# Kernel tuning notes

Measured on AMD Instinct MI355X. Metric: run time of the kernel, lower is better.

The kernel has to match this reference:

```python
import jax, jax.numpy as jnp
import numpy as np

N_NODES = 100000
N_EDGES = 1600000
D_IN, D_HID, D_LAT = 128, 128, 64


def setup_inputs() -> dict:
    key = jax.random.key(0)
    ks = jax.random.split(key, 8)
    x = jax.random.normal(ks[0], (N_NODES, D_IN), dtype=jnp.float32)
    edge_index = jax.random.randint(ks[1], (2, N_EDGES), 0, N_NODES, dtype=jnp.int64)
    s1 = 1.0 / np.sqrt(D_IN)
    s2 = 1.0 / np.sqrt(D_HID)
    return {
        "x": x,
        "edge_index": edge_index,
        "W1_l": jax.random.normal(ks[2], (D_IN, D_HID), dtype=jnp.float32) * s1,
        "W1_r": jax.random.normal(ks[3], (D_IN, D_HID), dtype=jnp.float32) * s1,
        "b1": jnp.zeros((D_HID,), dtype=jnp.float32),
        "W2_l": jax.random.normal(ks[4], (D_HID, D_LAT), dtype=jnp.float32) * s2,
        "W2_r": jax.random.normal(ks[5], (D_HID, D_LAT), dtype=jnp.float32) * s2,
        "b2": jnp.zeros((D_LAT,), dtype=jnp.float32),
    }


def _sage_conv_mean(x, src, dst, W_l, W_r, b):
    """PyG SAGEConv with mean aggregation: lin_l(mean_j x_j) + lin_r(x_i)."""
    n = x.shape[0]
    # scatter-mean of source features into destination nodes
    agg = jax.ops.segment_sum(x[src], dst, num_segments=n)           # [N, d]
    deg = jax.ops.segment_sum(jnp.ones_like(dst, dtype=x.dtype), dst, num_segments=n)
    mean = agg / jnp.maximum(deg, 1.0)[:, None]
    return mean @ W_l + b + x @ W_r


def reference(x, edge_index, W1_l, W1_r, b1, W2_l, W2_r, b2):
    src, dst = edge_index[0], edge_index[1]
    h = jax.nn.relu(_sage_conv_mean(x, src, dst, W1_l, W1_r, b1))
    # Dropout(p=0.2) is identity in eval mode
    z = jax.nn.relu(_sage_conv_mean(h, src, dst, W2_l, W2_r, b2))
    return z
```

## Files before the change

kernel.cpp:

```cpp
#include <hip/hip_runtime.h>

#define N_NODES 100000
#define N_EDGES 1600000
#define D_IN 128
#define D_HID 128
#define D_LAT 64

#define BSHIFT 8
#define NB 392
#define CAP 4608
#define EPB 4096
#define PART_BLOCKS ((N_EDGES + EPB - 1) / EPB)
#define CVT_BLOCKS (((long)N_NODES * 128 / 16 + 255) / 256)

typedef unsigned short ushort_t;
typedef unsigned int uint_t;
typedef unsigned char uchar_t;
using bf16x8 = __attribute__((ext_vector_type(8))) short;
using f32x4  = __attribute__((ext_vector_type(4))) float;
using f32x2  = __attribute__((ext_vector_type(2))) float;

__device__ inline ushort_t f2bf(float f) {
    uint_t u = __float_as_uint(f);
    return (ushort_t)((u + 0x7fffu + ((u >> 16) & 1u)) >> 16);
}
__device__ inline uint_t pack2bf(float a, float b) {
    return (uint_t)f2bf(a) | ((uint_t)f2bf(b) << 16);
}
__device__ inline float bf2f(ushort_t u) {
    return __uint_as_float(((uint_t)u) << 16);
}

#if __has_builtin(__builtin_amdgcn_cvt_pk_f32_fp8) && __has_builtin(__builtin_amdgcn_cvt_pk_fp8_f32)
#define HW_FP8 1
template<bool HI>
__device__ inline f32x2 fp8pk2f(uint_t v) {
    return __builtin_amdgcn_cvt_pk_f32_fp8(v, HI);
}
__device__ inline uint_t f2fp8pk4(float a, float b, float c, float d) {
    uint_t w = __builtin_amdgcn_cvt_pk_fp8_f32(a, b, 0, false);
    w = __builtin_amdgcn_cvt_pk_fp8_f32(c, d, w, true);
    return w;
}
__device__ inline uchar_t f2fp8_byte(float f) {
    return (uchar_t)(__builtin_amdgcn_cvt_pk_fp8_f32(f, f, 0, false) & 0xff);
}
#else
__device__ inline float fp8b2f(uint_t b) {
    uint_t em = b & 0x7f;
    if (em == 0) return 0.f;
    uint_t bits = ((em << 20) + (120u << 23)) | ((b & 0x80u) << 24);
    return __uint_as_float(bits);
}
template<bool HI>
__device__ inline f32x2 fp8pk2f(uint_t v) {
    uint_t w = HI ? (v >> 16) : v;
    f32x2 r; r.x = fp8b2f(w & 0xff); r.y = fp8b2f((w >> 8) & 0xff);
    return r;
}
__device__ inline uint_t f2fp8_1(float f) {
    uint_t u = __float_as_uint(f);
    uint_t s = (u >> 31) << 7;
    uint_t au = u & 0x7fffffff;
    if (au >= 0x43e00000u) return s | 0x7e;
    if (au < 0x3c000000u) return s;
    uint_t r = au + 0x0007ffffu + ((au >> 20) & 1u);
    return s | (((r >> 20) - (120u << 3)) & 0x7f);
}
__device__ inline uint_t f2fp8pk4(float a, float b, float c, float d) {
    return f2fp8_1(a) | (f2fp8_1(b) << 8) | (f2fp8_1(c) << 16) | (f2fp8_1(d) << 24);
}
__device__ inline uchar_t f2fp8_byte(float f) { return (uchar_t)f2fp8_1(f); }
#endif

__device__ inline void accf8x4(float* a, uint_t w, int base) {
    f32x2 p0 = fp8pk2f<false>(w);
    f32x2 p1 = fp8pk2f<true>(w);
    a[base + 0] += p0.x; a[base + 1] += p0.y;
    a[base + 2] += p1.x; a[base + 3] += p1.y;
}
__device__ inline void accf8x16(float* a, uint4 u) {
    accf8x4(a, u.x, 0); accf8x4(a, u.y, 4); accf8x4(a, u.z, 8); accf8x4(a, u.w, 12);
}

template<int RSHIFT>
__device__ inline void gather_acc_fp8(const uchar_t* __restrict__ base,
                                      const int* __restrict__ idxp,
                                      int n, float* acc) {
    int k = 0;
    int idx[8];
    if (n >= 8) {
        #pragma unroll
        for (int j = 0; j < 8; ++j) idx[j] = idxp[j];
    }
    while (k + 8 <= n) {
        uint4 u[8];
        #pragma unroll
        for (int j = 0; j < 8; ++j)
            u[j] = *(const uint4*)(base + ((long)idx[j] << RSHIFT));
        int kn = k + 8;
        if (kn + 8 <= n) {
            #pragma unroll
            for (int j = 0; j < 8; ++j) idx[j] = idxp[kn + j];
        }
        #pragma unroll
        for (int j = 0; j < 8; ++j) accf8x16(acc, u[j]);
        k = kn;
    }
    if (k < n) {
        int m = n - k;
        int idr[8];
        #pragma unroll
        for (int j = 0; j < 8; ++j) {
            int kk = k + j; if (kk > n - 1) kk = n - 1;
            idr[j] = idxp[kk];
        }
        uint4 u[8];
        #pragma unroll
        for (int j = 0; j < 8; ++j)
            u[j] = *(const uint4*)(base + ((long)idr[j] << RSHIFT));
        #pragma unroll
        for (int j = 0; j < 8; ++j) if (j < m) accf8x16(acc, u[j]);
    }
}

__device__ inline void pack_w256(const float* Wl, const float* Wr, ushort_t* pack,
                                 int N, int tid) {
    int lane = tid & 63;
    int t = tid >> 6;
    int kt = t & 7;
    int nt = t >> 3;
    int n = nt * 16 + (lane & 15);
    int kbase = kt * 32 + (lane >> 4) * 8;
    ushort_t v[8];
    #pragma unroll
    for (int j = 0; j < 8; ++j) {
        int k = kbase + j;
        float w = (k < 128) ? Wl[k * N + n] : Wr[(k - 128) * N + n];
        v[j] = f2bf(w);
    }
    *(uint4*)(pack + (long)tid * 8) = *(uint4*)v;
}
__device__ inline void pack_w128(const float* W, ushort_t* pack, int N, int tid) {
    int lane = tid & 63;
    int t = tid >> 6;
    int kt = t & 3;
    int nt = t >> 2;
    int n = nt * 16 + (lane & 15);
    int kbase = kt * 32 + (lane >> 4) * 8;
    ushort_t v[8];
    #pragma unroll
    for (int j = 0; j < 8; ++j) v[j] = f2bf(W[(kbase + j) * N + n]);
    *(uint4*)(pack + (long)tid * 8) = *(uint4*)v;
}

__global__ __launch_bounds__(256) void prep_kernel(
        const float* __restrict__ W1_l, const float* __restrict__ W1_r,
        ushort_t* __restrict__ pack1,
        const float* __restrict__ W2_l, ushort_t* __restrict__ pack2l,
        const float* __restrict__ W2_r, ushort_t* __restrict__ pack2r,
        int* __restrict__ gCur,
        const float* __restrict__ x, ushort_t* __restrict__ xb,
        uchar_t* __restrict__ x8) {
    int b = blockIdx.x;
    if (b < 16) {
        pack_w256(W1_l, W1_r, pack1, 128, b * 256 + threadIdx.x);
    } else if (b < 20) {
        pack_w128(W2_l, pack2l, 64, (b - 16) * 256 + threadIdx.x);
    } else if (b < 24) {
        pack_w128(W2_r, pack2r, 64, (b - 20) * 256 + threadIdx.x);
    } else if (b < 26) {
        int t = (b - 24) * 256 + threadIdx.x;
        if (t < NB) gCur[t] = t * CAP;
    } else {
        long i = ((long)(b - 26) * 256 + threadIdx.x) * 16;
        if (i >= (long)N_NODES * 128) return;
        float4 a = *(const float4*)(x + i);
        float4 bb = *(const float4*)(x + i + 4);
        float4 c = *(const float4*)(x + i + 8);
        float4 d = *(const float4*)(x + i + 12);
        uint4 ob0, ob1;
        ob0.x = pack2bf(a.x, a.y);  ob0.y = pack2bf(a.z, a.w);
        ob0.z = pack2bf(bb.x, bb.y); ob0.w = pack2bf(bb.z, bb.w);
        ob1.x = pack2bf(c.x, c.y);  ob1.y = pack2bf(c.z, c.w);
        ob1.z = pack2bf(d.x, d.y);  ob1.w = pack2bf(d.z, d.w);
        *(uint4*)(xb + i) = ob0;
        *(uint4*)(xb + i + 8) = ob1;
        uint4 o8;
        o8.x = f2fp8pk4(a.x, a.y, a.z, a.w);
        o8.y = f2fp8pk4(bb.x, bb.y, bb.z, bb.w);
        o8.z = f2fp8pk4(c.x, c.y, c.z, c.w);
        o8.w = f2fp8pk4(d.x, d.y, d.z, d.w);
        *(uint4*)(x8 + i) = o8;
    }
}

__global__ __launch_bounds__(256) void bucket_scatter_kernel(const int* __restrict__ src,
                                                             const int* __restrict__ dst,
                                                             int* __restrict__ gCur,
                                                             int* __restrict__ bedges) {
    __shared__ int h[NB];
    __shared__ int start[NB];
    for (int j = threadIdx.x; j < NB; j += 256) h[j] = 0;
    __syncthreads();
    long base = (long)blockIdx.x * EPB + threadIdx.x * 16;
    int dc[16], sc[16];
    int cnt = 0;
    if (base + 16 <= N_EDGES) {
        #pragma unroll
        for (int j = 0; j < 4; ++j) {
            int4 d4 = *(const int4*)(dst + base + j * 4);
            int4 s4 = *(const int4*)(src + base + j * 4);
            dc[j * 4 + 0] = d4.x; dc[j * 4 + 1] = d4.y; dc[j * 4 + 2] = d4.z; dc[j * 4 + 3] = d4.w;
            sc[j * 4 + 0] = s4.x; sc[j * 4 + 1] = s4.y; sc[j * 4 + 2] = s4.z; sc[j * 4 + 3] = s4.w;
        }
        cnt = 16;
    } else if (base < N_EDGES) {
        cnt = (int)(N_EDGES - base);
        for (int j = 0; j < cnt; ++j) { dc[j] = dst[base + j]; sc[j] = src[base + j]; }
    }
    for (int j = 0; j < cnt; ++j) atomicAdd(&h[dc[j] >> BSHIFT], 1);
    __syncthreads();
    for (int j = threadIdx.x; j < NB; j += 256)
        start[j] = h[j] ? atomicAdd(&gCur[j], h[j]) : 0;
    __syncthreads();
    for (int j = 0; j < cnt; ++j) {
        int b = dc[j] >> BSHIFT;
        int p = atomicAdd(&start[b], 1);
        if (p < (b + 1) * CAP)
            bedges[p] = ((dc[j] & 255) << 24) | sc[j];
    }
}

__global__ __launch_bounds__(256) void bucket_sort_kernel(const int* __restrict__ gCur,
                                                          const int* __restrict__ bedges,
                                                          int* __restrict__ csr,
                                                          int2* __restrict__ off2) {
    __shared__ int sdata[256];
    __shared__ int cur[256];
    int b = blockIdx.x, t = threadIdx.x;
    int r0 = b * CAP;
    int n = gCur[b] - r0;
    if (n > CAP) n = CAP;
    cur[t] = 0;
    __syncthreads();
    for (int k = t * 4; k < n; k += 1024) {
        int4 v4 = *(const int4*)(bedges + r0 + k);
        int m = n - k;
        atomicAdd(&cur[(unsigned)v4.x >> 24], 1);
        if (m > 1) atomicAdd(&cur[(unsigned)v4.y >> 24], 1);
        if (m > 2) atomicAdd(&cur[(unsigned)v4.z >> 24], 1);
        if (m > 3) atomicAdd(&cur[(unsigned)v4.w >> 24], 1);
    }
    __syncthreads();
    int c = cur[t];
    sdata[t] = c;
    __syncthreads();
    for (int d = 1; d < 256; d <<= 1) {
        int u = (t >= d) ? sdata[t - d] : 0;
        __syncthreads();
        sdata[t] += u;
        __syncthreads();
    }
    int ex = (t == 0) ? 0 : sdata[t - 1];
    off2[(b << BSHIFT) + t] = make_int2(r0 + ex, c);
    cur[t] = ex;
    __syncthreads();
    for (int k = t * 4; k < n; k += 1024) {
        int4 v4 = *(const int4*)(bedges + r0 + k);
        int m = n - k;
        {
            int p = atomicAdd(&cur[(unsigned)v4.x >> 24], 1);
            csr[r0 + p] = v4.x & 0xFFFFFF;
        }
        if (m > 1) {
            int p = atomicAdd(&cur[(unsigned)v4.y >> 24], 1);
            csr[r0 + p] = v4.y & 0xFFFFFF;
        }
        if (m > 2) {
            int p = atomicAdd(&cur[(unsigned)v4.z >> 24], 1);
            csr[r0 + p] = v4.z & 0xFFFFFF;
        }
        if (m > 3) {
            int p = atomicAdd(&cur[(unsigned)v4.w >> 24], 1);
            csr[r0 + p] = v4.w & 0xFFFFFF;
        }
    }
}

__global__ __launch_bounds__(256) void gather_mean_fp8_kernel(
        const int2* __restrict__ off2, const int* __restrict__ csr_src,
        const uchar_t* __restrict__ x8, ushort_t* __restrict__ mean_out) {
    int lane  = threadIdx.x & 7;
    int local = threadIdx.x >> 3;
    long i = (long)blockIdx.x * 32 + local;
    if (i >= N_NODES) return;
    int2 bd = off2[i];
    int beg = bd.x, n = bd.y;
    const uchar_t* base = x8 + lane * 16;
    float acc[16];
    #pragma unroll
    for (int j = 0; j < 16; ++j) acc[j] = 0.f;
    gather_acc_fp8<7>(base, csr_src + beg, n, acc);
    float inv = (n > 0) ? 1.f / (float)n : 0.f;
    uint4 o0, o1;
    o0.x = pack2bf(acc[0] * inv,  acc[1] * inv);
    o0.y = pack2bf(acc[2] * inv,  acc[3] * inv);
    o0.z = pack2bf(acc[4] * inv,  acc[5] * inv);
    o0.w = pack2bf(acc[6] * inv,  acc[7] * inv);
    o1.x = pack2bf(acc[8] * inv,  acc[9] * inv);
    o1.y = pack2bf(acc[10] * inv, acc[11] * inv);
    o1.z = pack2bf(acc[12] * inv, acc[13] * inv);
    o1.w = pack2bf(acc[14] * inv, acc[15] * inv);
    ushort_t* mp = mean_out + i * 128 + lane * 16;
    *(uint4*)mp = o0;
    *(uint4*)(mp + 8) = o1;
}

#define HSTRIDE 132
__global__ __launch_bounds__(256) void mfma_mlp_fused_kernel(
        const ushort_t* __restrict__ Am, const ushort_t* __restrict__ Ax,
        const ushort_t* __restrict__ pack1, const float* __restrict__ bias,
        const ushort_t* __restrict__ pack2l,
        ushort_t* __restrict__ hb, uchar_t* __restrict__ g8) {
    __shared__ ushort_t htile[4][16 * HSTRIDE];
    int lane = threadIdx.x & 63;
    int wave = threadIdx.x >> 6;
    long m0 = (long)blockIdx.x * 64 + wave * 16;
    int r = lane & 15;
    int quad = lane >> 4;
    long arow = m0 + r;
    if (arow > N_NODES - 1) arow = N_NODES - 1;

    bf16x8 areg[8];
    #pragma unroll
    for (int kt = 0; kt < 8; ++kt) {
        const ushort_t* s = (kt < 4) ? Am : Ax;
        int k = (kt & 3) * 32 + quad * 8;
        areg[kt] = *(const bf16x8*)(s + arow * 128 + k);
    }

    f32x4 acc[8];
    #pragma unroll
    for (int nt = 0; nt < 8; ++nt) acc[nt] = (f32x4){0.f, 0.f, 0.f, 0.f};
    #pragma unroll
    for (int nt = 0; nt < 8; ++nt) {
        #pragma unroll
        for (int kt = 0; kt < 8; ++kt) {
            bf16x8 bfrag = *(const bf16x8*)(pack1 + ((long)(nt * 8 + kt) * 64 + lane) * 8);
            acc[nt] = __builtin_amdgcn_mfma_f32_16x16x32_bf16(areg[kt], bfrag, acc[nt], 0, 0, 0);
        }
    }

    #pragma unroll
    for (int nt = 0; nt < 8; ++nt) {
        int col = nt * 16 + r;
        float bj = bias[col];
        #pragma unroll
        for (int q = 0; q < 4; ++q) {
            long orow = m0 + quad * 4 + q;
            float v = fmaxf(acc[nt][q] + bj, 0.f);
            ushort_t hv = f2bf(v);
            if (orow < N_NODES) hb[orow * 128 + col] = hv;
            htile[wave][(quad * 4 + q) * HSTRIDE + col] = hv;
        }
    }
    bf16x8 areg2[4];
    #pragma unroll
    for (int kt = 0; kt < 4; ++kt)
        areg2[kt] = *(const bf16x8*)(&htile[wave][r * HSTRIDE + kt * 32 + quad * 8]);
    f32x4 gacc[4];
    #pragma unroll
    for (int nt = 0; nt < 4; ++nt) gacc[nt] = (f32x4){0.f, 0.f, 0.f, 0.f};
    #pragma unroll
    for (int nt = 0; nt < 4; ++nt) {
        #pragma unroll
        for (int kt = 0; kt < 4; ++kt) {
            bf16x8 bfrag = *(const bf16x8*)(pack2l + ((long)(nt * 4 + kt) * 64 + lane) * 8);
            gacc[nt] = __builtin_amdgcn_mfma_f32_16x16x32_bf16(areg2[kt], bfrag, gacc[nt], 0, 0, 0);
        }
    }
    #pragma unroll
    for (int nt = 0; nt < 4; ++nt) {
        int col = nt * 16 + r;
        #pragma unroll
        for (int q = 0; q < 4; ++q) {
            long orow = m0 + quad * 4 + q;
            if (orow < N_NODES) g8[orow * 64 + col] = f2fp8_byte(gacc[nt][q]);
        }
    }
}

#define MSTRIDE 68
__global__ __launch_bounds__(256) void mfma_final_kernel(
        const int2* __restrict__ off2, const int* __restrict__ csr_src,
        const uchar_t* __restrict__ g8,
        const ushort_t* __restrict__ hb, const ushort_t* __restrict__ pack2r,
        const float* __restrict__ b2, float* __restrict__ out) {
    __shared__ ushort_t mtile[64 * MSTRIDE];
    long m0 = (long)blockIdx.x * 64;
    {
        int lane  = threadIdx.x & 3;
        int local = threadIdx.x >> 2;
        long i = m0 + local;
        if (i > N_NODES - 1) i = N_NODES - 1;
        int2 bd = off2[i];
        int beg = bd.x, n = bd.y;
        const uchar_t* base = g8 + lane * 16;
        float acc[16];
        #pragma unroll
        for (int j = 0; j < 16; ++j) acc[j] = 0.f;
        gather_acc_fp8<6>(base, csr_src + beg, n, acc);
        float inv = (n > 0) ? 1.f / (float)n : 0.f;
        uint4 o0, o1;
        o0.x = pack2bf(acc[0] * inv,  acc[1] * inv);
        o0.y = pack2bf(acc[2] * inv,  acc[3] * inv);
        o0.z = pack2bf(acc[4] * inv,  acc[5] * inv);
        o0.w = pack2bf(acc[6] * inv,  acc[7] * inv);
        o1.x = pack2bf(acc[8] * inv,  acc[9] * inv);
        o1.y = pack2bf(acc[10] * inv, acc[11] * inv);
        o1.z = pack2bf(acc[12] * inv, acc[13] * inv);
        o1.w = pack2bf(acc[14] * inv, acc[15] * inv);
        ushort_t* mp = mtile + local * MSTRIDE + lane * 16;
        *(uint4*)mp = o0;
        *(uint4*)(mp + 8) = o1;
    }
    __syncthreads();
    int lane = threadIdx.x & 63;
    int wave = threadIdx.x >> 6;
    long mw = m0 + wave * 16;
    int r = lane & 15;
    int quad = lane >> 4;
    long arow = mw + r;
    if (arow > N_NODES - 1) arow = N_NODES - 1;

    bf16x8 areg[4];
    #pragma unroll
    for (int kt = 0; kt < 4; ++kt)
        areg[kt] = *(const bf16x8*)(hb + arow * 128 + kt * 32 + quad * 8);

    f32x4 acc[4];
    #pragma unroll
    for (int nt = 0; nt < 4; ++nt) {
        int col = nt * 16 + r;
        #pragma unroll
        for (int q = 0; q < 4; ++q) {
            int rowl = wave * 16 + quad * 4 + q;
            acc[nt][q] = bf2f(mtile[rowl * MSTRIDE + col]);
        }
    }
    #pragma unroll
    for (int nt = 0; nt < 4; ++nt) {
        #pragma unroll
        for (int kt = 0; kt < 4; ++kt) {
            bf16x8 bfrag = *(const bf16x8*)(pack2r + ((long)(nt * 4 + kt) * 64 + lane) * 8);
            acc[nt] = __builtin_amdgcn_mfma_f32_16x16x32_bf16(areg[kt], bfrag, acc[nt], 0, 0, 0);
        }
    }
    #pragma unroll
    for (int nt = 0; nt < 4; ++nt) {
        int col = nt * 16 + r;
        float bj = b2[col];
        #pragma unroll
        for (int q = 0; q < 4; ++q) {
            long orow = mw + quad * 4 + q;
            if (orow < N_NODES)
                out[orow * 64 + col] = fmaxf(acc[nt][q] + bj, 0.f);
        }
    }
}

extern "C" void kernel_launch(void* const* d_in, const int* in_sizes, int n_in,
                              void* d_out, int out_size, void* d_ws, size_t ws_size,
                              hipStream_t stream) {
    const float* x    = (const float*)d_in[0];
    const int*   ei   = (const int*)d_in[1];
    const float* W1_l = (const float*)d_in[2];
    const float* W1_r = (const float*)d_in[3];
    const float* b1   = (const float*)d_in[4];
    const float* W2_l = (const float*)d_in[5];
    const float* W2_r = (const float*)d_in[6];
    const float* b2   = (const float*)d_in[7];
    float* out = (float*)d_out;

    const int* src = ei;
    const int* dst = ei + N_EDGES;

    int*  gCur   = (int*)d_ws;
    int2* off2   = (int2*)(gCur + 512);
    int*  bedges = (int*)(off2 + 100608);
    int*  csr    = bedges + NB * CAP;
    ushort_t* xb    = (ushort_t*)(csr + NB * CAP);
    ushort_t* mean1 = xb + (long)N_NODES * 128;
    ushort_t* hb    = mean1 + (long)N_NODES * 128;
    uchar_t*  x8    = (uchar_t*)hb;
    ushort_t* pack1  = hb + (long)N_NODES * 128;
    ushort_t* pack2l = pack1 + 256 * 128;
    ushort_t* pack2r = pack2l + 128 * 64;
    uchar_t*  g8     = (uchar_t*)(pack2r + 128 * 64);

    prep_kernel<<<26 + CVT_BLOCKS, 256, 0, stream>>>(
        W1_l, W1_r, pack1, W2_l, pack2l, W2_r, pack2r, gCur, x, xb, x8);

    bucket_scatter_kernel<<<PART_BLOCKS, 256, 0, stream>>>(src, dst, gCur, bedges);
    bucket_sort_kernel<<<NB, 256, 0, stream>>>(gCur, bedges, csr, off2);

    gather_mean_fp8_kernel<<<(N_NODES + 31) / 32, 256, 0, stream>>>(off2, csr, x8, mean1);
    mfma_mlp_fused_kernel<<<(N_NODES + 63) / 64, 256, 0, stream>>>(
        mean1, xb, pack1, b1, pack2l, hb, g8);

    mfma_final_kernel<<<(N_NODES + 63) / 64, 256, 0, stream>>>(
        off2, csr, g8, hb, pack2r, b2, out);
}
```

Before: 242.6 us.

## Fuse layer-1 neighbor gather-mean into the MFMA MLP kernel via shared memory

Removes the standalone gather-mean kernel and computes each block's 64 node means inside the fused MFMA kernel, staging them in LDS rather than writing and rereading a bf16 mean buffer in global memory. Each node now uses 4 lanes covering 32 features, with two 16-byte loads per neighbor at depth 4. This saves one launch and about 25 MB of global write plus read, in exchange for more registers and LDS per block, which may lower occupancy of the gather phase. The gather helper is generalized by vector count and depth, and the final kernel keeps its previous 8-deep, single-vector setting.

```diff
diff --git a/kernel.cpp b/kernel.cpp
--- a/kernel.cpp
+++ b/kernel.cpp
@@ -83,44 +83,60 @@
     accf8x4(a, u.x, 0); accf8x4(a, u.y, 4); accf8x4(a, u.z, 8); accf8x4(a, u.w, 12);
 }
 
-template<int RSHIFT>
-__device__ inline void gather_acc_fp8(const uchar_t* __restrict__ base,
-                                      const int* __restrict__ idxp,
-                                      int n, float* acc) {
+template<int RSHIFT, int NV, int DEPTH>
+__device__ inline void gather_acc_fp8n(const uchar_t* __restrict__ base,
+                                       const int* __restrict__ idxp,
+                                       int n, float* acc) {
     int k = 0;
-    int idx[8];
-    if (n >= 8) {
-        #pragma unroll
-        for (int j = 0; j < 8; ++j) idx[j] = idxp[j];
-    }
-    while (k + 8 <= n) {
-        uint4 u[8];
-        #pragma unroll
-        for (int j = 0; j < 8; ++j)
-            u[j] = *(const uint4*)(base + ((long)idx[j] << RSHIFT));
-        int kn = k + 8;
-        if (kn + 8 <= n) {
+    int idx[DEPTH];
+    if (n >= DEPTH) {
+        #pragma unroll
+        for (int j = 0; j < DEPTH; ++j) idx[j] = idxp[j];
+    }
+    while (k + DEPTH <= n) {
+        uint4 u[DEPTH][NV];
+        #pragma unroll
+        for (int j = 0; j < DEPTH; ++j) {
             #pragma unroll
-            for (int j = 0; j < 8; ++j) idx[j] = idxp[kn + j];
-        }
-        #pragma unroll
-        for (int j = 0; j < 8; ++j) accf8x16(acc, u[j]);
+            for (int v = 0; v < NV; ++v)
+                u[j][v] = *(const uint4*)(base + ((long)idx[j] << RSHIFT) + v * 16);
+        }
+        int kn = k + DEPTH;
+        if (kn + DEPTH <= n) {
+            #pragma unroll
+            for (int j = 0; j < DEPTH; ++j) idx[j] = idxp[kn + j];
+        }
+        #pragma unroll
+        for (int j = 0; j < DEPTH; ++j) {
+            #pragma unroll
+            for (int v = 0; v < NV; ++v)
+                accf8x16(acc + v * 16, u[j][v]);
+        }
         k = kn;
     }
     if (k < n) {
         int m = n - k;
-        int idr[8];
-        #pragma unroll
-        for (int j = 0; j < 8; ++j) {
+        int idr[DEPTH];
+        #pragma unroll
+        for (int j = 0; j < DEPTH; ++j) {
             int kk = k + j; if (kk > n - 1) kk = n - 1;
             idr[j] = idxp[kk];
         }
-        uint4 u[8];
-        #pragma unroll
-        for (int j = 0; j < 8; ++j)
-            u[j] = *(const uint4*)(base + ((long)idr[j] << RSHIFT));
-        #pragma unroll
-        for (int j = 0; j < 8; ++j) if (j < m) accf8x16(acc, u[j]);
+        uint4 u[DEPTH][NV];
+        #pragma unroll
+        for (int j = 0; j < DEPTH; ++j) {
+            #pragma unroll
+            for (int v = 0; v < NV; ++v)
+                u[j][v] = *(const uint4*)(base + ((long)idr[j] << RSHIFT) + v * 16);
+        }
+        #pragma unroll
+        for (int j = 0; j < DEPTH; ++j) {
+            if (j < m) {
+                #pragma unroll
+                for (int v = 0; v < NV; ++v)
+                    accf8x16(acc + v * 16, u[j][v]);
+            }
+        }
     }
 }
 
@@ -288,56 +304,60 @@
     }
 }
 
-__global__ __launch_bounds__(256) void gather_mean_fp8_kernel(
-        const int2* __restrict__ off2, const int* __restrict__ csr_src,
-        const uchar_t* __restrict__ x8, ushort_t* __restrict__ mean_out) {
-    int lane  = threadIdx.x & 7;
-    int local = threadIdx.x >> 3;
-    long i = (long)blockIdx.x * 32 + local;
-    if (i >= N_NODES) return;
-    int2 bd = off2[i];
-    int beg = bd.x, n = bd.y;
-    const uchar_t* base = x8 + lane * 16;
-    float acc[16];
-    #pragma unroll
-    for (int j = 0; j < 16; ++j) acc[j] = 0.f;
-    gather_acc_fp8<7>(base, csr_src + beg, n, acc);
-    float inv = (n > 0) ? 1.f / (float)n : 0.f;
-    uint4 o0, o1;
-    o0.x = pack2bf(acc[0] * inv,  acc[1] * inv);
-    o0.y = pack2bf(acc[2] * inv,  acc[3] * inv);
-    o0.z = pack2bf(acc[4] * inv,  acc[5] * inv);
-    o0.w = pack2bf(acc[6] * inv,  acc[7] * inv);
-    o1.x = pack2bf(acc[8] * inv,  acc[9] * inv);
-    o1.y = pack2bf(acc[10] * inv, acc[11] * inv);
-    o1.z = pack2bf(acc[12] * inv, acc[13] * inv);
-    o1.w = pack2bf(acc[14] * inv, acc[15] * inv);
-    ushort_t* mp = mean_out + i * 128 + lane * 16;
-    *(uint4*)mp = o0;
-    *(uint4*)(mp + 8) = o1;
-}
-
 #define HSTRIDE 132
 __global__ __launch_bounds__(256) void mfma_mlp_fused_kernel(
-        const ushort_t* __restrict__ Am, const ushort_t* __restrict__ Ax,
+        const int2* __restrict__ off2, const int* __restrict__ csr_src,
+        const uchar_t* __restrict__ x8,
+        const ushort_t* __restrict__ Ax,
         const ushort_t* __restrict__ pack1, const float* __restrict__ bias,
         const ushort_t* __restrict__ pack2l,
         ushort_t* __restrict__ hb, uchar_t* __restrict__ g8) {
+    __shared__ ushort_t mtile[64 * HSTRIDE];
     __shared__ ushort_t htile[4][16 * HSTRIDE];
+    long m0b = (long)blockIdx.x * 64;
+    {
+        int lane4 = threadIdx.x & 3;
+        int local = threadIdx.x >> 2;
+        long i = m0b + local;
+        if (i > N_NODES - 1) i = N_NODES - 1;
+        int2 bd = off2[i];
+        const uchar_t* gbase = x8 + lane4 * 32;
+        float acc[32];
+        #pragma unroll
+        for (int j = 0; j < 32; ++j) acc[j] = 0.f;
+        gather_acc_fp8n<7, 2, 4>(gbase, csr_src + bd.x, bd.y, acc);
+        float inv = (bd.y > 0) ? 1.f / (float)bd.y : 0.f;
+        uint_t o[8];
+        #pragma unroll
+        for (int j = 0; j < 8; ++j)
+            o[j] = pack2bf(acc[j * 2] * inv, acc[j * 2 + 1] * inv);
+        ushort_t* mp = mtile + local * HSTRIDE + lane4 * 32;
+        *(uint4*)mp = *(uint4*)o;
+        *(uint4*)(mp + 8) = *(uint4*)(o + 4);
+        uint_t o2[8];
+        #pragma unroll
+        for (int j = 0; j < 8; ++j)
+            o2[j] = pack2bf(acc[16 + j * 2] * inv, acc[16 + j * 2 + 1] * inv);
+        *(uint4*)(mp + 16) = *(uint4*)o2;
+        *(uint4*)(mp + 24) = *(uint4*)(o2 + 4);
+    }
+    __syncthreads();
     int lane = threadIdx.x & 63;
     int wave = threadIdx.x >> 6;
-    long m0 = (long)blockIdx.x * 64 + wave * 16;
+    long m0 = m0b + wave * 16;
     int r = lane & 15;
     int quad = lane >> 4;
     long arow = m0 + r;
     if (arow > N_NODES - 1) arow = N_NODES - 1;
+    int rowl = wave * 16 + r;
 
     bf16x8 areg[8];
     #pragma unroll
     for (int kt = 0; kt < 8; ++kt) {
-        const ushort_t* s = (kt < 4) ? Am : Ax;
         int k = (kt & 3) * 32 + quad * 8;
-        areg[kt] = *(const bf16x8*)(s + arow * 128 + k);
+        areg[kt] = (kt < 4)
+            ? *(const bf16x8*)(&mtile[rowl * HSTRIDE + k])
+            : *(const bf16x8*)(Ax + arow * 128 + k);
     }
 
     f32x4 acc[8];
@@ -410,7 +430,7 @@
         float acc[16];
         #pragma unroll
         for (int j = 0; j < 16; ++j) acc[j] = 0.f;
-        gather_acc_fp8<6>(base, csr_src + beg, n, acc);
+        gather_acc_fp8n<6, 1, 8>(base, csr_src + beg, n, acc);
         float inv = (n > 0) ? 1.f / (float)n : 0.f;
         uint4 o0, o1;
         o0.x = pack2bf(acc[0] * inv,  acc[1] * inv);
@@ -490,11 +510,10 @@
     int2* off2   = (int2*)(gCur + 512);
     int*  bedges = (int*)(off2 + 100608);
     int*  csr    = bedges + NB * CAP;
-    ushort_t* xb    = (ushort_t*)(csr + NB * CAP);
-    ushort_t* mean1 = xb + (long)N_NODES * 128;
-    ushort_t* hb    = mean1 + (long)N_NODES * 128;
-    uchar_t*  x8    = (uchar_t*)hb;
-    ushort_t* pack1  = hb + (long)N_NODES * 128;
+    ushort_t* xb = (ushort_t*)(csr + NB * CAP);
+    ushort_t* hb = xb + (long)N_NODES * 128;
+    uchar_t*  x8 = (uchar_t*)(hb + (long)N_NODES * 128);
+    ushort_t* pack1  = (ushort_t*)(x8 + (long)N_NODES * 128);
     ushort_t* pack2l = pack1 + 256 * 128;
     ushort_t* pack2r = pack2l + 128 * 64;
     uchar_t*  g8     = (uchar_t*)(pack2r + 128 * 64);
@@ -505,9 +524,8 @@
     bucket_scatter_kernel<<<PART_BLOCKS, 256, 0, stream>>>(src, dst, gCur, bedges);
     bucket_sort_kernel<<<NB, 256, 0, stream>>>(gCur, bedges, csr, off2);
 
-    gather_mean_fp8_kernel<<<(N_NODES + 31) / 32, 256, 0, stream>>>(off2, csr, x8, mean1);
     mfma_mlp_fused_kernel<<<(N_NODES + 63) / 64, 256, 0, stream>>>(
-        mean1, xb, pack1, b1, pack2l, hb, g8);
+        off2, csr, x8, xb, pack1, b1, pack2l, hb, g8);
 
     mfma_final_kernel<<<(N_NODES + 63) / 64, 256, 0, stream>>>(
         off2, csr, g8, hb, pack2r, b2, out);
```

Result: slower. 256.6 us (+5.8%).
